# Kernel tuning notes

Hardware: AMD Instinct MI355X
Metric: run time of the kernel (lower is better)

Reference implementation:

```python
import jax, jax.numpy as jnp
import numpy as np

H, KVH, D = 32, 8, 128
HID = H * D
OP = H * D + 2 * KVH * D
T = 2048
LAYER_IDX = 8
LAMBDA_INIT = float(0.8 - 0.6 * np.exp(-0.3 * LAYER_IDX))
EPS = 1e-5


def setup_inputs() -> dict:
    key = jax.random.key(0)
    ks = jax.random.split(key, 10)
    s = 0.02
    return {
        "hidden_states": jax.random.normal(ks[0], (T, HID), jnp.float32),
        "wqkv_w": jax.random.normal(ks[1], (OP, HID), jnp.float32) * s,
        "wqkv_b": jax.random.normal(ks[2], (OP,), jnp.float32) * s,
        "lambda_q1": jax.random.normal(ks[3], (D,), jnp.float32) * 0.1,
        "lambda_k1": jax.random.normal(ks[4], (D,), jnp.float32) * 0.1,
        "lambda_q2": jax.random.normal(ks[5], (D,), jnp.float32) * 0.1,
        "lambda_k2": jax.random.normal(ks[6], (D,), jnp.float32) * 0.1,
        "subln_w": jnp.ones((2 * D,), jnp.float32),
        "out_w": jax.random.normal(ks[7], (HID, HID), jnp.float32) * s,
        "out_b": jax.random.normal(ks[8], (HID,), jnp.float32) * s,
    }


def reference(hidden_states, wqkv_w, wqkv_b, lambda_q1, lambda_k1,
              lambda_q2, lambda_k2, subln_w, out_w, out_b):
    t = hidden_states.shape[0]
    scale = D ** -0.5

    qkv = hidden_states @ wqkv_w.T + wqkv_b                     # [T, OP]
    q, k, v = jnp.split(qkv, [H * D, H * D + KVH * D], axis=-1)

    # pair-wise head split: consecutive heads form (pair, component) groups
    q = q.reshape(t, H // 2, 2, D)                              # [T, Hp, 2, D]
    k = k.reshape(t, KVH // 2, 2, D)                            # [T, KVHp, 2, D]
    v = v.reshape(t, KVH // 2, 2 * D)                           # [T, KVHp, 2D]

    rep = H // KVH  # GQA: query pair p -> kv pair p // rep
    k = jnp.repeat(k, rep, axis=1)                              # [T, Hp, 2, D]
    v = jnp.repeat(v, rep, axis=1)                              # [T, Hp, 2D]

    lam = (jnp.exp(jnp.dot(lambda_q1, lambda_k1))
           - jnp.exp(jnp.dot(lambda_q2, lambda_k2)) + LAMBDA_INIT)

    causal = jnp.tril(jnp.ones((t, t), bool))
    scores = jnp.einsum('qhcd,khcd->hcqk', q, k) * scale        # [Hp, 2, T, T]
    scores = jnp.where(causal, scores, -jnp.inf)
    probs = jax.nn.softmax(scores, axis=-1)
    attn = probs[:, 0] - lam * probs[:, 1]                      # [Hp, T, T]

    out = jnp.einsum('hqk,khd->qhd', attn, v)                   # [T, Hp, 2D]

    # per-head RMSNorm over 2D, scaled by (1 - lambda_init)
    rms = jax.lax.rsqrt(jnp.mean(out * out, axis=-1, keepdims=True) + EPS)
    out = out * rms * subln_w * (1.0 - LAMBDA_INIT)

    out = out.reshape(t, H * D)
    return out @ out_w.T + out_b
```

## Files before the change

### kernel.cpp

```cpp
#include <hip/hip_runtime.h>

#define TTOK 2048
#define HIDN 4096
#define OPD  6144
#define DH   128
#define VD   256
#define KOFF 4096
#define VOFF 5120

typedef short  s16x8 __attribute__((ext_vector_type(8)));
typedef unsigned short u16x8 __attribute__((ext_vector_type(8)));
typedef float  fx4   __attribute__((ext_vector_type(4)));

constexpr float LAM_INIT = 0.7455692280263534f;
constexpr float OML      = 1.0f - LAM_INIT;
constexpr float QKSCALE  = 0.08838834764831845f;
constexpr float RESCALE_THR = 8.0f;

__device__ __forceinline__ unsigned short f2bf(float f) {
  unsigned int u = __builtin_bit_cast(unsigned int, f);
  u += 0x7fffu + ((u >> 16) & 1u);
  return (unsigned short)(u >> 16);
}

__device__ __forceinline__ void g2l16(const void* gsrc, void* ldst) {
  __builtin_amdgcn_global_load_lds(
      (const __attribute__((address_space(1))) unsigned int*)gsrc,
      (__attribute__((address_space(3))) unsigned int*)ldst, 16, 0, 0);
}

__global__ __launch_bounds__(256)
void cvt3(const float* __restrict__ s0, unsigned short* __restrict__ d0, int nb0,
          const float* __restrict__ s1, unsigned short* __restrict__ d1, int nb1,
          const float* __restrict__ s2, unsigned short* __restrict__ d2)
{
  const int b = blockIdx.x;
  const float* s; unsigned short* d; int base;
  if (b < nb0)            { s = s0; d = d0; base = b << 11; }
  else if (b < nb0 + nb1) { s = s1; d = d1; base = (b - nb0) << 11; }
  else                    { s = s2; d = d2; base = (b - nb0 - nb1) << 11; }
  const int i = base + (int)threadIdx.x * 8;
  const float4 a0 = *(const float4*)(s + i);
  const float4 a1 = *(const float4*)(s + i + 4);
  u16x8 v;
  v[0]=f2bf(a0.x); v[1]=f2bf(a0.y); v[2]=f2bf(a0.z); v[3]=f2bf(a0.w);
  v[4]=f2bf(a1.x); v[5]=f2bf(a1.y); v[6]=f2bf(a1.z); v[7]=f2bf(a1.w);
  *(u16x8*)(d + i) = v;
}

template<int MW, bool QKVOUT, bool OUTBF16>
__global__ __launch_bounds__(512, 2)
void gemm_8ph(const unsigned short* __restrict__ A, const unsigned short* __restrict__ B,
              const float* __restrict__ bias, void* __restrict__ Cp,
              unsigned short* __restrict__ ctt, int K, int lda, int ldb, int ldc)
{
  constexpr int BM   = MW * 32;
  constexpr int MH   = MW / 2;
  constexpr int ALD2 = MW / 4;
  __shared__ __align__(16) unsigned short As[2][2][(BM / 2) * 64];
  __shared__ __align__(16) unsigned short Bs[2][2][128 * 64];

  const int tid  = threadIdx.x;
  const int lane = tid & 63, wid = tid >> 6;
  const int wm = wid >> 2, wn = wid & 3;
  const int m0 = blockIdx.y * BM, n0 = blockIdx.x * 256;
  const int l15 = lane & 15, lg = lane >> 4;

  const int srow = tid >> 3;
  const int scol = ((tid & 7) ^ ((tid >> 3) & 7)) << 3;
  const int rsw = (l15 & 7) << 3;
  const int ck0 = (lg * 8) ^ rsw;
  const int ck1 = (32 + lg * 8) ^ rsw;
  const int arh = wm * 16 + l15;
  const int brh = wn * 16 + l15;

  auto stageAh = [&](int kt, int buf, int h) {
    #pragma unroll
    for (int i = 0; i < ALD2; ++i)
      g2l16(A + (size_t)(m0 + h * (BM / 2) + i * 64 + srow) * lda + kt + scol,
            &As[buf][h][(i * 512 + tid) * 8]);
  };
  auto stageBh = [&](int kt, int buf, int h) {
    #pragma unroll
    for (int i = 0; i < 2; ++i)
      g2l16(B + (size_t)(n0 + h * 128 + i * 64 + srow) * ldb + kt + scol,
            &Bs[buf][h][(i * 512 + tid) * 8]);
  };

  fx4 acc[MW][4] = {};

  const int nk = K >> 6;
  stageAh(0, 0, 0); stageBh(0, 0, 0); stageBh(0, 0, 1); stageAh(0, 0, 1);
  asm volatile("s_waitcnt vmcnt(0)" ::: "memory");
  __builtin_amdgcn_s_barrier();

  for (int t = 0; t < nk; ++t) {
    const int buf = t & 1, nb = buf ^ 1;
    const int kt1 = (t + 1) << 6;
    const bool pre = (t + 1) < nk;
    const unsigned short* A0 = &As[buf][0][0];
    const unsigned short* A1 = &As[buf][1][0];
    const unsigned short* B0 = &Bs[buf][0][0];
    const unsigned short* B1 = &Bs[buf][1][0];
    s16x8 af[MH][2], bf[2][2];

    #pragma unroll
    for (int m = 0; m < MH; ++m) {
      af[m][0] = *(const s16x8*)&A0[(arh + m * 32) * 64 + ck0];
      af[m][1] = *(const s16x8*)&A0[(arh + m * 32) * 64 + ck1];
    }
    #pragma unroll
    for (int n = 0; n < 2; ++n) {
      bf[n][0] = *(const s16x8*)&B0[(brh + n * 64) * 64 + ck0];
      bf[n][1] = *(const s16x8*)&B0[(brh + n * 64) * 64 + ck1];
    }
    if (pre) {
      stageAh(kt1, nb, 0);
      if constexpr (MW == 8) asm volatile("s_waitcnt vmcnt(4)" ::: "memory");
      else                   asm volatile("s_waitcnt vmcnt(2)" ::: "memory");
    } else {
      asm volatile("s_waitcnt vmcnt(0)" ::: "memory");
    }
    __builtin_amdgcn_s_barrier();
    __builtin_amdgcn_s_setprio(1);
    #pragma unroll
    for (int m = 0; m < MH; ++m)
      #pragma unroll
      for (int n = 0; n < 2; ++n) {
        acc[m][n] = __builtin_amdgcn_mfma_f32_16x16x32_bf16(af[m][0], bf[n][0], acc[m][n], 0, 0, 0);
        acc[m][n] = __builtin_amdgcn_mfma_f32_16x16x32_bf16(af[m][1], bf[n][1], acc[m][n], 0, 0, 0);
      }
    __builtin_amdgcn_s_setprio(0);

    #pragma unroll
    for (int n = 0; n < 2; ++n) {
      bf[n][0] = *(const s16x8*)&B1[(brh + n * 64) * 64 + ck0];
      bf[n][1] = *(const s16x8*)&B1[(brh + n * 64) * 64 + ck1];
    }
    if (pre) {
      stageBh(kt1, nb, 0);
      if constexpr (MW == 8) asm volatile("s_waitcnt vmcnt(4)" ::: "memory");
      else                   asm volatile("s_waitcnt vmcnt(3)" ::: "memory");
    }
    __builtin_amdgcn_s_barrier();
    __builtin_amdgcn_s_setprio(1);
    #pragma unroll
    for (int m = 0; m < MH; ++m)
      #pragma unroll
      for (int n = 0; n < 2; ++n) {
        acc[m][2 + n] = __builtin_amdgcn_mfma_f32_16x16x32_bf16(af[m][0], bf[n][0], acc[m][2 + n], 0, 0, 0);
        acc[m][2 + n] = __builtin_amdgcn_mfma_f32_16x16x32_bf16(af[m][1], bf[n][1], acc[m][2 + n], 0, 0, 0);
      }
    __builtin_amdgcn_s_setprio(0);

    #pragma unroll
    for (int m = 0; m < MH; ++m) {
      af[m][0] = *(const s16x8*)&A1[(arh + m * 32) * 64 + ck0];
      af[m][1] = *(const s16x8*)&A1[(arh + m * 32) * 64 + ck1];
    }
    if (pre) stageBh(kt1, nb, 1);
    __builtin_amdgcn_s_setprio(1);
    #pragma unroll
    for (int m = 0; m < MH; ++m)
      #pragma unroll
      for (int n = 0; n < 2; ++n) {
        acc[MH + m][2 + n] = __builtin_amdgcn_mfma_f32_16x16x32_bf16(af[m][0], bf[n][0], acc[MH + m][2 + n], 0, 0, 0);
        acc[MH + m][2 + n] = __builtin_amdgcn_mfma_f32_16x16x32_bf16(af[m][1], bf[n][1], acc[MH + m][2 + n], 0, 0, 0);
      }
    __builtin_amdgcn_s_setprio(0);

    #pragma unroll
    for (int n = 0; n < 2; ++n) {
      bf[n][0] = *(const s16x8*)&B0[(brh + n * 64) * 64 + ck0];
      bf[n][1] = *(const s16x8*)&B0[(brh + n * 64) * 64 + ck1];
    }
    if (pre) {
      stageAh(kt1, nb, 1);
      if constexpr (MW == 8) asm volatile("s_waitcnt vmcnt(4)" ::: "memory");
      else                   asm volatile("s_waitcnt vmcnt(3)" ::: "memory");
    }
    __builtin_amdgcn_s_barrier();
    __builtin_amdgcn_s_setprio(1);
    #pragma unroll
    for (int m = 0; m < MH; ++m)
      #pragma unroll
      for (int n = 0; n < 2; ++n) {
        acc[MH + m][n] = __builtin_amdgcn_mfma_f32_16x16x32_bf16(af[m][0], bf[n][0], acc[MH + m][n], 0, 0, 0);
        acc[MH + m][n] = __builtin_amdgcn_mfma_f32_16x16x32_bf16(af[m][1], bf[n][1], acc[MH + m][n], 0, 0, 0);
      }
    __builtin_amdgcn_s_setprio(0);
  }

  const int rb = m0 + wm * 16;
  const int cb = n0 + wn * 16;
  if (QKVOUT && n0 >= VOFF) {
    #pragma unroll
    for (int mi = 0; mi < MW; ++mi)
      #pragma unroll
      for (int ni = 0; ni < 4; ++ni) {
        const int col = cb + ni * 64 + l15;
        const float bv = bias[col];
        const fx4 a = acc[mi][ni];
        ushort4 pk;
        pk.x = f2bf(a[0] + bv); pk.y = f2bf(a[1] + bv);
        pk.z = f2bf(a[2] + bv); pk.w = f2bf(a[3] + bv);
        const int d   = col - VOFF;
        const int kvp = d >> 8, dw = d & 255;
        const int row0 = rb + mi * 32 + lg * 4;
        const int kt2 = row0 >> 5, kk = row0 & 31;
        const int kc = kk >> 3, k8 = kk & 7;
        *(ushort4*)&ctt[(size_t)kvp * 1048576 + (size_t)kt2 * 16384 + 8192
                        + kc * 2048 + dw * 8 + k8] = pk;
      }
  } else if (QKVOUT && n0 >= KOFF) {
    #pragma unroll
    for (int mi = 0; mi < MW; ++mi)
      #pragma unroll
      for (int ni = 0; ni < 4; ++ni) {
        const int col = cb + ni * 64 + l15;
        const int ccol = col - KOFF;
        const float bv = bias[col];
        const int kvp = ccol >> 8, cw = ccol & 255;
        const int cc = cw >> 3, cbt = cw & 7;
        const fx4 a = acc[mi][ni];
        #pragma unroll
        for (int jj = 0; jj < 4; ++jj) {
          const int row2 = rb + mi * 32 + lg * 4 + jj;
          const int kt2 = row2 >> 5, kk = row2 & 31;
          ctt[(size_t)kvp * 1048576 + (size_t)kt2 * 16384 + cc * 256 + kk * 8 + cbt]
              = f2bf(a[jj] + bv);
        }
      }
  } else {
    #pragma unroll
    for (int mi = 0; mi < MW; ++mi)
      #pragma unroll
      for (int ni = 0; ni < 4; ++ni) {
        const int col = cb + ni * 64 + l15;
        const float bv = bias[col];
        const fx4 a = acc[mi][ni];
        #pragma unroll
        for (int jj = 0; jj < 4; ++jj) {
          const int row2 = rb + mi * 32 + lg * 4 + jj;
          const float v = a[jj] + bv;
          if (OUTBF16) ((unsigned short*)Cp)[(size_t)row2 * ldc + col] = f2bf(v);
          else         ((float*)Cp)[(size_t)row2 * ldc + col] = v;
        }
      }
  }
}

__global__ __launch_bounds__(256, 2)
void attn_kernel(const unsigned short* __restrict__ qq,
                 const unsigned short* __restrict__ ctt,
                 const float* __restrict__ lq1, const float* __restrict__ lk1,
                 const float* __restrict__ lq2, const float* __restrict__ lk2,
                 const float* __restrict__ subln,
                 unsigned short* __restrict__ attn_out)
{
  __shared__ __align__(16) unsigned short Sb[2][16384];
  __shared__ __align__(16) unsigned short Pl[4][2][640];
  const int tid = threadIdx.x;
  const int lane = tid & 63, w = tid >> 6;
  const int l15 = lane & 15, lg = lane >> 4;

  const int bid = blockIdx.x;
  const int g = bid & 7, s = bid >> 3;
  const int kvp  = g >> 1;
  const int pair = kvp * 4 + (s & 3);
  const int qb   = 31 - ((s >> 2) << 1) - (g & 1);
  const int q0b  = qb * 64;
  const int q0w  = q0b + w * 16;
  const int nt   = 2 * qb + 2;

  const unsigned short* cbase = ctt + (size_t)kvp * 1048576;

  auto stage = [&](int kt, int buf) {
    const unsigned short* src = cbase + (size_t)kt * 16384;
    const int off = w * 512 + lane * 8;
    #pragma unroll
    for (int i = 0; i < 8; ++i) {
      const int o = i * 2048 + off;
      g2l16(src + o, &Sb[buf][o]);
    }
  };

  stage(0, 0);

  float a1 = lq1[lane] * lk1[lane] + lq1[lane + 64] * lk1[lane + 64];
  float a2 = lq2[lane] * lk2[lane] + lq2[lane + 64] * lk2[lane + 64];
  #pragma unroll
  for (int sft = 1; sft < 64; sft <<= 1) { a1 += __shfl_xor(a1, sft); a2 += __shfl_xor(a2, sft); }
  const float lam = __expf(a1) - __expf(a2) + LAM_INIT;

  s16x8 qf0[4], qf1[4];
  {
    const unsigned short* qbp = qq + (size_t)(q0w + l15) * HIDN + pair * VD + lg * 8;
    #pragma unroll
    for (int kf = 0; kf < 4; ++kf) {
      qf0[kf] = *(const s16x8*)(qbp + kf * 32);
      qf1[kf] = *(const s16x8*)(qbp + DH + kf * 32);
    }
  }

  float mrun0 = -1e30f, mrun1 = -1e30f;
  float lrun0 = 0.f, lrun1 = 0.f;
  fx4 oacc0[16] = {}, oacc1[16] = {};
  unsigned short* pl0 = &Pl[w][0][0];
  unsigned short* pl1 = &Pl[w][1][0];
  const int q = q0w + l15;
  const int qmax = q0w + 15;

  for (int t = 0; t < nt; ++t) {
    __syncthreads();
    if (t + 1 < nt) stage(t + 1, (t + 1) & 1);
    const int kb = t * 32;
    if (kb > qmax) continue;
    const unsigned short* Kl = Sb[t & 1];
    const unsigned short* Vl = Sb[t & 1] + 8192;

    fx4 s00 = {0,0,0,0}, s01 = {0,0,0,0}, s10 = {0,0,0,0}, s11 = {0,0,0,0};
    #pragma unroll
    for (int kf = 0; kf < 4; ++kf) {
      const int cc0 = kf * 4 + lg;
      const int cc1 = 16 + kf * 4 + lg;
      const s16x8 k00 = *(const s16x8*)&Kl[cc0 * 256 + l15 * 8];
      const s16x8 k01 = *(const s16x8*)&Kl[cc0 * 256 + (16 + l15) * 8];
      const s16x8 k10 = *(const s16x8*)&Kl[cc1 * 256 + l15 * 8];
      const s16x8 k11 = *(const s16x8*)&Kl[cc1 * 256 + (16 + l15) * 8];
      s00 = __builtin_amdgcn_mfma_f32_16x16x32_bf16(k00, qf0[kf], s00, 0, 0, 0);
      s01 = __builtin_amdgcn_mfma_f32_16x16x32_bf16(k01, qf0[kf], s01, 0, 0, 0);
      s10 = __builtin_amdgcn_mfma_f32_16x16x32_bf16(k10, qf1[kf], s10, 0, 0, 0);
      s11 = __builtin_amdgcn_mfma_f32_16x16x32_bf16(k11, qf1[kf], s11, 0, 0, 0);
    }

    float v0[8], v1[8];
    #pragma unroll
    for (int j = 0; j < 4; ++j) {
      const int klo = kb + lg * 4 + j, khi = klo + 16;
      v0[j]     = (klo <= q) ? s00[j] * QKSCALE : -1e30f;
      v0[4 + j] = (khi <= q) ? s01[j] * QKSCALE : -1e30f;
      v1[j]     = (klo <= q) ? s10[j] * QKSCALE : -1e30f;
      v1[4 + j] = (khi <= q) ? s11[j] * QKSCALE : -1e30f;
    }
    float tm0 = fmaxf(fmaxf(fmaxf(v0[0],v0[1]),fmaxf(v0[2],v0[3])),
                      fmaxf(fmaxf(v0[4],v0[5]),fmaxf(v0[6],v0[7])));
    float tm1 = fmaxf(fmaxf(fmaxf(v1[0],v1[1]),fmaxf(v1[2],v1[3])),
                      fmaxf(fmaxf(v1[4],v1[5]),fmaxf(v1[6],v1[7])));
    tm0 = fmaxf(tm0, __shfl_xor(tm0, 16)); tm0 = fmaxf(tm0, __shfl_xor(tm0, 32));
    tm1 = fmaxf(tm1, __shfl_xor(tm1, 16)); tm1 = fmaxf(tm1, __shfl_xor(tm1, 32));

    const bool need = (tm0 > mrun0 + RESCALE_THR) || (tm1 > mrun1 + RESCALE_THR);
    if (__any(need)) {
      const float mn0 = fmaxf(mrun0, tm0), mn1 = fmaxf(mrun1, tm1);
      const float fac0 = __expf(mrun0 - mn0), fac1 = __expf(mrun1 - mn1);
      mrun0 = mn0; mrun1 = mn1;
      lrun0 *= fac0; lrun1 *= fac1;
      #pragma unroll
      for (int jj = 0; jj < 4; ++jj) {
        const float fr0 = __shfl(fac0, lg * 4 + jj);
        const float fr1 = __shfl(fac1, lg * 4 + jj);
        #pragma unroll
        for (int nf = 0; nf < 16; ++nf) { oacc0[nf][jj] *= fr0; oacc1[nf][jj] *= fr1; }
      }
    }

    {
      float ps0 = 0.f, ps1 = 0.f;
      ushort4 lo0, hi0, lo1, hi1;
      float p;
      p = __expf(v0[0]-mrun0); ps0 += p; lo0.x = f2bf(p);
      p = __expf(v0[1]-mrun0); ps0 += p; lo0.y = f2bf(p);
      p = __expf(v0[2]-mrun0); ps0 += p; lo0.z = f2bf(p);
      p = __expf(v0[3]-mrun0); ps0 += p; lo0.w = f2bf(p);
      p = __expf(v0[4]-mrun0); ps0 += p; hi0.x = f2bf(p);
      p = __expf(v0[5]-mrun0); ps0 += p; hi0.y = f2bf(p);
      p = __expf(v0[6]-mrun0); ps0 += p; hi0.z = f2bf(p);
      p = __expf(v0[7]-mrun0); ps0 += p; hi0.w = f2bf(p);
      p = __expf(v1[0]-mrun1); ps1 += p; lo1.x = f2bf(p);
      p = __expf(v1[1]-mrun1); ps1 += p; lo1.y = f2bf(p);
      p = __expf(v1[2]-mrun1); ps1 += p; lo1.z = f2bf(p);
      p = __expf(v1[3]-mrun1); ps1 += p; lo1.w = f2bf(p);
      p = __expf(v1[4]-mrun1); ps1 += p; hi1.x = f2bf(p);
      p = __expf(v1[5]-mrun1); ps1 += p; hi1.y = f2bf(p);
      p = __expf(v1[6]-mrun1); ps1 += p; hi1.z = f2bf(p);
      p = __expf(v1[7]-mrun1); ps1 += p; hi1.w = f2bf(p);
      lrun0 += ps0; lrun1 += ps1;
      *(ushort4*)&pl0[l15 * 40 + lg * 4]      = lo0;
      *(ushort4*)&pl0[l15 * 40 + 16 + lg * 4] = hi0;
      *(ushort4*)&pl1[l15 * 40 + lg * 4]      = lo1;
      *(ushort4*)&pl1[l15 * 40 + 16 + lg * 4] = hi1;
    }
    asm volatile("s_waitcnt lgkmcnt(0)" ::: "memory");
    __builtin_amdgcn_sched_barrier(0);

    const s16x8 pa0 = *(const s16x8*)&pl0[l15 * 40 + lg * 8];
    const s16x8 pa1 = *(const s16x8*)&pl1[l15 * 40 + lg * 8];
    #pragma unroll
    for (int nf = 0; nf < 16; ++nf) {
      const s16x8 vf = *(const s16x8*)&Vl[lg * 2048 + (nf * 16 + l15) * 8];
      oacc0[nf] = __builtin_amdgcn_mfma_f32_16x16x32_bf16(pa0, vf, oacc0[nf], 0, 0, 0);
      oacc1[nf] = __builtin_amdgcn_mfma_f32_16x16x32_bf16(pa1, vf, oacc1[nf], 0, 0, 0);
    }
  }

  lrun0 += __shfl_xor(lrun0, 16); lrun0 += __shfl_xor(lrun0, 32);
  lrun1 += __shfl_xor(lrun1, 16); lrun1 += __shfl_xor(lrun1, 32);

  float li0[4], li1[4];
  #pragma unroll
  for (int jj = 0; jj < 4; ++jj) {
    li0[jj] = 1.0f / __shfl(lrun0, lg * 4 + jj);
    li1[jj] = 1.0f / __shfl(lrun1, lg * 4 + jj);
  }

  float ss[4] = {0.f, 0.f, 0.f, 0.f};
  #pragma unroll
  for (int nf = 0; nf < 16; ++nf)
    #pragma unroll
    for (int jj = 0; jj < 4; ++jj) {
      const float o = oacc0[nf][jj] * li0[jj] - lam * oacc1[nf][jj] * li1[jj];
      oacc0[nf][jj] = o;
      ss[jj] += o * o;
    }
  #pragma unroll
  for (int jj = 0; jj < 4; ++jj) {
    ss[jj] += __shfl_xor(ss[jj], 1);
    ss[jj] += __shfl_xor(ss[jj], 2);
    ss[jj] += __shfl_xor(ss[jj], 4);
    ss[jj] += __shfl_xor(ss[jj], 8);
    ss[jj] = rsqrtf(ss[jj] * (1.0f / 256.0f) + 1e-5f) * OML;
  }
  #pragma unroll
  for (int nf = 0; nf < 16; ++nf) {
    const int dcol = nf * 16 + l15;
    const float sw = subln[dcol];
    #pragma unroll
    for (int jj = 0; jj < 4; ++jj) {
      const int t = q0w + lg * 4 + jj;
      attn_out[(size_t)t * HIDN + pair * VD + dcol] = f2bf(oacc0[nf][jj] * ss[jj] * sw);
    }
  }
}

extern "C" void kernel_launch(void* const* d_in, const int* in_sizes, int n_in,
                              void* d_out, int out_size, void* d_ws, size_t ws_size,
                              hipStream_t stream) {
  (void)in_sizes; (void)n_in; (void)out_size; (void)ws_size;
  const float* hs     = (const float*)d_in[0];
  const float* wqkv_w = (const float*)d_in[1];
  const float* wqkv_b = (const float*)d_in[2];
  const float* lq1    = (const float*)d_in[3];
  const float* lk1    = (const float*)d_in[4];
  const float* lq2    = (const float*)d_in[5];
  const float* lk2    = (const float*)d_in[6];
  const float* subln  = (const float*)d_in[7];
  const float* out_w  = (const float*)d_in[8];
  const float* out_b  = (const float*)d_in[9];

  unsigned short* qq       = (unsigned short*)d_ws;
  unsigned short* ctt      = qq + (size_t)TTOK * HIDN;
  unsigned short* attn_out = ctt + (size_t)4 * 1048576;
  unsigned short* hs_bf    = attn_out + (size_t)TTOK * HIDN;
  unsigned short* wqkv_bf  = hs_bf + (size_t)TTOK * HIDN;
  unsigned short* outw_bf  = wqkv_bf + (size_t)OPD * HIDN;

  const int nb0 = (TTOK * HIDN) >> 11;
  const int nb1 = (OPD * HIDN) >> 11;
  const int nb2 = (HIDN * HIDN) >> 11;
  cvt3<<<dim3(nb0 + nb1 + nb2), 256, 0, stream>>>(
      hs, hs_bf, nb0, wqkv_w, wqkv_bf, nb1, out_w, outw_bf);

  gemm_8ph<8, true, true><<<dim3(OPD / 256, TTOK / 256), 512, 0, stream>>>(
      hs_bf, wqkv_bf, wqkv_b, qq, ctt, HIDN, HIDN, HIDN, HIDN);

  attn_kernel<<<dim3(512), 256, 0, stream>>>(
      qq, ctt, lq1, lk1, lq2, lk2, subln, attn_out);

  gemm_8ph<4, false, false><<<dim3(HIDN / 256, TTOK / 128), 512, 0, stream>>>(
      attn_out, outw_bf, out_b, d_out, nullptr, HIDN, HIDN, HIDN, HIDN);
}
```

Baseline: 357.1 us.

## Split-K out-projection with larger tiles and keep B fragments in registers

The output projection GEMM now uses 256x256 tiles with a split-K of 2. Each K-half writes fp32 partials into reused workspace, and a new reduce kernel sums them and adds the bias. The main GEMM loop keeps two sets of B fragments in registers, so the final phase no longer reloads B0 from LDS, and the last waitcnt/barrier moves after that phase's MFMAs. The aim is better data reuse and less LDS traffic, at the cost of extra global traffic for the partials and one more kernel launch.

```diff
diff --git a/kernel.cpp b/kernel.cpp
--- a/kernel.cpp
+++ b/kernel.cpp
@@ -48,7 +48,22 @@
   *(u16x8*)(d + i) = v;
 }
 
-template<int MW, bool QKVOUT, bool OUTBF16>
+__global__ __launch_bounds__(256)
+void reduce2(const float* __restrict__ p, const float* __restrict__ bias,
+             float* __restrict__ out)
+{
+  const size_t i = ((size_t)blockIdx.x * 256 + threadIdx.x) * 4;
+  const int col = (int)(i & (HIDN - 1));
+  const float4 a = *(const float4*)(p + i);
+  const float4 b = *(const float4*)(p + (size_t)TTOK * HIDN + i);
+  const float4 c = *(const float4*)(bias + col);
+  float4 r;
+  r.x = a.x + b.x + c.x; r.y = a.y + b.y + c.y;
+  r.z = a.z + b.z + c.z; r.w = a.w + b.w + c.w;
+  *(float4*)(out + i) = r;
+}
+
+template<int MW, int MODE>
 __global__ __launch_bounds__(512, 2)
 void gemm_8ph(const unsigned short* __restrict__ A, const unsigned short* __restrict__ B,
               const float* __restrict__ bias, void* __restrict__ Cp,
@@ -65,6 +80,7 @@
   const int wm = wid >> 2, wn = wid & 3;
   const int m0 = blockIdx.y * BM, n0 = blockIdx.x * 256;
   const int l15 = lane & 15, lg = lane >> 4;
+  const int kOff = (MODE == 1) ? blockIdx.z * K : 0;
 
   const int srow = tid >> 3;
   const int scol = ((tid & 7) ^ ((tid >> 3) & 7)) << 3;
@@ -77,13 +93,13 @@
   auto stageAh = [&](int kt, int buf, int h) {
     #pragma unroll
     for (int i = 0; i < ALD2; ++i)
-      g2l16(A + (size_t)(m0 + h * (BM / 2) + i * 64 + srow) * lda + kt + scol,
+      g2l16(A + (size_t)(m0 + h * (BM / 2) + i * 64 + srow) * lda + kOff + kt + scol,
             &As[buf][h][(i * 512 + tid) * 8]);
   };
   auto stageBh = [&](int kt, int buf, int h) {
     #pragma unroll
     for (int i = 0; i < 2; ++i)
-      g2l16(B + (size_t)(n0 + h * 128 + i * 64 + srow) * ldb + kt + scol,
+      g2l16(B + (size_t)(n0 + h * 128 + i * 64 + srow) * ldb + kOff + kt + scol,
             &Bs[buf][h][(i * 512 + tid) * 8]);
   };
 
@@ -102,7 +118,7 @@
     const unsigned short* A1 = &As[buf][1][0];
     const unsigned short* B0 = &Bs[buf][0][0];
     const unsigned short* B1 = &Bs[buf][1][0];
-    s16x8 af[MH][2], bf[2][2];
+    s16x8 af[MH][2], bf0[2][2], bf1[2][2];
 
     #pragma unroll
     for (int m = 0; m < MH; ++m) {
@@ -111,13 +127,12 @@
     }
     #pragma unroll
     for (int n = 0; n < 2; ++n) {
-      bf[n][0] = *(const s16x8*)&B0[(brh + n * 64) * 64 + ck0];
-      bf[n][1] = *(const s16x8*)&B0[(brh + n * 64) * 64 + ck1];
+      bf0[n][0] = *(const s16x8*)&B0[(brh + n * 64) * 64 + ck0];
+      bf0[n][1] = *(const s16x8*)&B0[(brh + n * 64) * 64 + ck1];
     }
     if (pre) {
       stageAh(kt1, nb, 0);
-      if constexpr (MW == 8) asm volatile("s_waitcnt vmcnt(4)" ::: "memory");
-      else                   asm volatile("s_waitcnt vmcnt(2)" ::: "memory");
+      asm volatile("s_waitcnt vmcnt(4)" ::: "memory");
     } else {
       asm volatile("s_waitcnt vmcnt(0)" ::: "memory");
     }
@@ -127,20 +142,19 @@
     for (int m = 0; m < MH; ++m)
       #pragma unroll
       for (int n = 0; n < 2; ++n) {
-        acc[m][n] = __builtin_amdgcn_mfma_f32_16x16x32_bf16(af[m][0], bf[n][0], acc[m][n], 0, 0, 0);
-        acc[m][n] = __builtin_amdgcn_mfma_f32_16x16x32_bf16(af[m][1], bf[n][1], acc[m][n], 0, 0, 0);
+        acc[m][n] = __builtin_amdgcn_mfma_f32_16x16x32_bf16(af[m][0], bf0[n][0], acc[m][n], 0, 0, 0);
+        acc[m][n] = __builtin_amdgcn_mfma_f32_16x16x32_bf16(af[m][1], bf0[n][1], acc[m][n], 0, 0, 0);
       }
     __builtin_amdgcn_s_setprio(0);
 
     #pragma unroll
     for (int n = 0; n < 2; ++n) {
-      bf[n][0] = *(const s16x8*)&B1[(brh + n * 64) * 64 + ck0];
-      bf[n][1] = *(const s16x8*)&B1[(brh + n * 64) * 64 + ck1];
+      bf1[n][0] = *(const s16x8*)&B1[(brh + n * 64) * 64 + ck0];
+      bf1[n][1] = *(const s16x8*)&B1[(brh + n * 64) * 64 + ck1];
     }
     if (pre) {
       stageBh(kt1, nb, 0);
-      if constexpr (MW == 8) asm volatile("s_waitcnt vmcnt(4)" ::: "memory");
-      else                   asm volatile("s_waitcnt vmcnt(3)" ::: "memory");
+      asm volatile("s_waitcnt vmcnt(4)" ::: "memory");
     }
     __builtin_amdgcn_s_barrier();
     __builtin_amdgcn_s_setprio(1);
@@ -148,8 +162,8 @@
     for (int m = 0; m < MH; ++m)
       #pragma unroll
       for (int n = 0; n < 2; ++n) {
-        acc[m][2 + n] = __builtin_amdgcn_mfma_f32_16x16x32_bf16(af[m][0], bf[n][0], acc[m][2 + n], 0, 0, 0);
-        acc[m][2 + n] = __builtin_amdgcn_mfma_f32_16x16x32_bf16(af[m][1], bf[n][1], acc[m][2 + n], 0, 0, 0);
+        acc[m][2 + n] = __builtin_amdgcn_mfma_f32_16x16x32_bf16(af[m][0], bf1[n][0], acc[m][2 + n], 0, 0, 0);
+        acc[m][2 + n] = __builtin_amdgcn_mfma_f32_16x16x32_bf16(af[m][1], bf1[n][1], acc[m][2 + n], 0, 0, 0);
       }
     __builtin_amdgcn_s_setprio(0);
 
@@ -164,36 +178,40 @@
     for (int m = 0; m < MH; ++m)
       #pragma unroll
       for (int n = 0; n < 2; ++n) {
-        acc[MH + m][2 + n] = __builtin_amdgcn_mfma_f32_16x16x32_bf16(af[m][0], bf[n][0], acc[MH + m][2 + n], 0, 0, 0);
-        acc[MH + m][2 + n] = __builtin_amdgcn_mfma_f32_16x16x32_bf16(af[m][1], bf[n][1], acc[MH + m][2 + n], 0, 0, 0);
+        acc[MH + m][2 + n] = __builtin_amdgcn_mfma_f32_16x16x32_bf16(af[m][0], bf1[n][0], acc[MH + m][2 + n], 0, 0, 0);
+        acc[MH + m][2 + n] = __builtin_amdgcn_mfma_f32_16x16x32_bf16(af[m][1], bf1[n][1], acc[MH + m][2 + n], 0, 0, 0);
       }
     __builtin_amdgcn_s_setprio(0);
 
-    #pragma unroll
-    for (int n = 0; n < 2; ++n) {
-      bf[n][0] = *(const s16x8*)&B0[(brh + n * 64) * 64 + ck0];
-      bf[n][1] = *(const s16x8*)&B0[(brh + n * 64) * 64 + ck1];
-    }
-    if (pre) {
-      stageAh(kt1, nb, 1);
-      if constexpr (MW == 8) asm volatile("s_waitcnt vmcnt(4)" ::: "memory");
-      else                   asm volatile("s_waitcnt vmcnt(3)" ::: "memory");
-    }
+    if (pre) stageAh(kt1, nb, 1);
+    __builtin_amdgcn_s_setprio(1);
+    #pragma unroll
+    for (int m = 0; m < MH; ++m)
+      #pragma unroll
+      for (int n = 0; n < 2; ++n) {
+        acc[MH + m][n] = __builtin_amdgcn_mfma_f32_16x16x32_bf16(af[m][0], bf0[n][0], acc[MH + m][n], 0, 0, 0);
+        acc[MH + m][n] = __builtin_amdgcn_mfma_f32_16x16x32_bf16(af[m][1], bf0[n][1], acc[MH + m][n], 0, 0, 0);
+      }
+    __builtin_amdgcn_s_setprio(0);
+    if (pre) asm volatile("s_waitcnt vmcnt(4)" ::: "memory");
     __builtin_amdgcn_s_barrier();
-    __builtin_amdgcn_s_setprio(1);
-    #pragma unroll
-    for (int m = 0; m < MH; ++m)
-      #pragma unroll
-      for (int n = 0; n < 2; ++n) {
-        acc[MH + m][n] = __builtin_amdgcn_mfma_f32_16x16x32_bf16(af[m][0], bf[n][0], acc[MH + m][n], 0, 0, 0);
-        acc[MH + m][n] = __builtin_amdgcn_mfma_f32_16x16x32_bf16(af[m][1], bf[n][1], acc[MH + m][n], 0, 0, 0);
-      }
-    __builtin_amdgcn_s_setprio(0);
   }
 
   const int rb = m0 + wm * 16;
   const int cb = n0 + wn * 16;
-  if (QKVOUT && n0 >= VOFF) {
+  if (MODE == 1) {
+    float* P = (float*)Cp + (size_t)blockIdx.z * (size_t)gridDim.y * BM * ldc;
+    #pragma unroll
+    for (int mi = 0; mi < MW; ++mi)
+      #pragma unroll
+      for (int ni = 0; ni < 4; ++ni) {
+        const int col = cb + ni * 64 + l15;
+        const fx4 a = acc[mi][ni];
+        #pragma unroll
+        for (int jj = 0; jj < 4; ++jj)
+          P[(size_t)(rb + mi * 32 + lg * 4 + jj) * ldc + col] = a[jj];
+      }
+  } else if (n0 >= VOFF) {
     #pragma unroll
     for (int mi = 0; mi < MW; ++mi)
       #pragma unroll
@@ -212,7 +230,7 @@
         *(ushort4*)&ctt[(size_t)kvp * 1048576 + (size_t)kt2 * 16384 + 8192
                         + kc * 2048 + dw * 8 + k8] = pk;
       }
-  } else if (QKVOUT && n0 >= KOFF) {
+  } else if (n0 >= KOFF) {
     #pragma unroll
     for (int mi = 0; mi < MW; ++mi)
       #pragma unroll
@@ -242,9 +260,7 @@
         #pragma unroll
         for (int jj = 0; jj < 4; ++jj) {
           const int row2 = rb + mi * 32 + lg * 4 + jj;
-          const float v = a[jj] + bv;
-          if (OUTBF16) ((unsigned short*)Cp)[(size_t)row2 * ldc + col] = f2bf(v);
-          else         ((float*)Cp)[(size_t)row2 * ldc + col] = v;
+          ((unsigned short*)Cp)[(size_t)row2 * ldc + col] = f2bf(a[jj] + bv);
         }
       }
   }
@@ -464,6 +480,7 @@
   unsigned short* hs_bf    = attn_out + (size_t)TTOK * HIDN;
   unsigned short* wqkv_bf  = hs_bf + (size_t)TTOK * HIDN;
   unsigned short* outw_bf  = wqkv_bf + (size_t)OPD * HIDN;
+  float*          partial  = (float*)hs_bf;
 
   const int nb0 = (TTOK * HIDN) >> 11;
   const int nb1 = (OPD * HIDN) >> 11;
@@ -471,12 +488,15 @@
   cvt3<<<dim3(nb0 + nb1 + nb2), 256, 0, stream>>>(
       hs, hs_bf, nb0, wqkv_w, wqkv_bf, nb1, out_w, outw_bf);
 
-  gemm_8ph<8, true, true><<<dim3(OPD / 256, TTOK / 256), 512, 0, stream>>>(
+  gemm_8ph<8, 0><<<dim3(OPD / 256, TTOK / 256), 512, 0, stream>>>(
       hs_bf, wqkv_bf, wqkv_b, qq, ctt, HIDN, HIDN, HIDN, HIDN);
 
   attn_kernel<<<dim3(512), 256, 0, stream>>>(
       qq, ctt, lq1, lk1, lq2, lk2, subln, attn_out);
 
-  gemm_8ph<4, false, false><<<dim3(HIDN / 256, TTOK / 128), 512, 0, stream>>>(
-      attn_out, outw_bf, out_b, d_out, nullptr, HIDN, HIDN, HIDN, HIDN);
-}
+  gemm_8ph<8, 1><<<dim3(HIDN / 256, TTOK / 256, 2), 512, 0, stream>>>(
+      attn_out, outw_bf, nullptr, partial, nullptr, HIDN / 2, HIDN, HIDN, HIDN);
+
+  reduce2<<<dim3((TTOK * HIDN) / 1024), 256, 0, stream>>>(
+      partial, out_b, (float*)d_out);
+}
```

Result: faster. 334.1 us (-6.4%).
